# Optimization experiments

Measured on AMD Instinct MI355X. Metric: run time of the kernel, lower is better.

## Reference

```python
import jax, jax.numpy as jnp
import numpy as np

# LLRDenoiser config (init_kwargs): ndim=2, patch W=8, stride S=4, ths=0.1, rand_shift=False
P = 8      # patch size (isotropic)
STRIDE = 4 # patch stride
THS = 0.1  # soft-threshold on singular values
B, C, H, W = 2, 16, 512, 512  # batch, coefficient axis, spatial dims


def setup_inputs() -> dict:
    key = jax.random.key(0)
    x = jax.random.normal(key, (B, C, H, W), dtype=jnp.float32)
    return {"x": x}


def _patch_idx(n, p, s):
    # start indices for sliding windows, inclusive of last full window
    starts = jnp.arange(0, n - p + 1, s)
    return starts[:, None] + jnp.arange(p)[None, :]  # (n_patches, p)


def _llr_denoise(x):
    idx_h = _patch_idx(H, P, STRIDE)  # (nH, P)
    idx_w = _patch_idx(W, P, STRIDE)  # (nW, P)
    nH, nW = idx_h.shape[0], idx_w.shape[0]
    hi = idx_h[:, None, :, None]  # (nH, 1, P, 1)
    wi = idx_w[None, :, None, :]  # (1, nW, 1, P)

    # extract overlapping patches -> (B, C, nH, nW, P, P)
    patches = x[:, :, hi, wi]
    # Casorati matrices per patch: (B, nH*nW, C, P*P)
    mats = patches.transpose(0, 2, 3, 1, 4, 5).reshape(B, nH * nW, C, P * P)

    # batched thin SVD + soft-threshold of singular values
    u, s, vh = jnp.linalg.svd(mats, full_matrices=False)
    s_st = jnp.sign(s) * jnp.maximum(jnp.abs(s) - THS, 0.0)
    mats = (u * s_st[..., None, :]) @ vh

    # back to patch layout (B, C, nH, nW, P, P)
    patches = mats.reshape(B, nH, nW, C, P, P).transpose(0, 3, 1, 2, 4, 5)

    # overlap-add reconstruction, averaged by patch coverage count
    out = jnp.zeros_like(x).at[:, :, hi, wi].add(patches)
    cnt = jnp.zeros((H, W), x.dtype).at[hi[..., 0, :, :] if False else idx_h[:, None, :, None], idx_w[None, :, None, :]].add(1.0)
    return out / cnt


def reference(x):
    return _llr_denoise(x)
```

## Files before the change

### kernel.cpp

```cpp
#include <hip/hip_runtime.h>


#define NBATCH  2
#define NCH     16
#define HDIM    512
#define WDIM    512
#define NPH     127
#define NPW     127
#define NPATCH  (NBATCH * NPH * NPW)
#define NCELL   128
#define THS     0.1f
#define NSIT    8

typedef short bf16x8 __attribute__((ext_vector_type(8)));
typedef float f32x4  __attribute__((ext_vector_type(4)));

#define MFMA(a,b,c) __builtin_amdgcn_mfma_f32_16x16x32_bf16((a),(b),(c),0,0,0)

static __device__ inline short f2bf(float x) {
  return __builtin_bit_cast(short, (__bf16)x);
}
static __device__ inline float blo2f(unsigned int v) {
  return __builtin_bit_cast(float, v << 16);
}
static __device__ inline float bhi2f(unsigned int v) {
  return __builtin_bit_cast(float, v & 0xffff0000u);
}
static __device__ inline unsigned int pack2bf(float lo, float hi) {
  unsigned int a = (unsigned short)f2bf(lo);
  unsigned int b = (unsigned short)f2bf(hi);
  return (b << 16) | a;
}

static __device__ inline int xcd_swz(int b, int nwg) {
  const int q = nwg >> 3, r = nwg & 7;
  const int x = b & 7, lo = b >> 3;
  return (x < r ? x * (q + 1) : r * (q + 1) + (x - r) * q) + lo;
}

static __device__ inline bf16x8 fragc(f32x4 v) {
  bf16x8 r;
  r[0] = f2bf(v[0]); r[1] = f2bf(v[1]); r[2] = f2bf(v[2]); r[3] = f2bf(v[3]);
  r[4] = 0; r[5] = 0; r[6] = 0; r[7] = 0;
  return r;
}

#define ZS_NBLK ((NPATCH + 3) / 4)
__global__ __launch_bounds__(256) void llr_zs(const float* __restrict__ x,
                                              uint2* __restrict__ zs) {
  const int blk = xcd_swz(blockIdx.x, ZS_NBLK);
  const int pid = blk * 4 + (threadIdx.x >> 6);
  if (pid >= NPATCH) return;
  const int bi  = pid / (NPH * NPW);
  const int pr  = pid % (NPH * NPW);
  const int ph  = pr / NPW, pw = pr % NPW;
  const int h0  = ph * 4, w0 = pw * 4;
  const int l   = threadIdx.x & 63;
  const int j   = l & 15;
  const int u   = l >> 4;

  const size_t HW = (size_t)HDIM * WDIM;
  const float* xb = x + (size_t)bi * NCH * HW;

  const float* pb = xb + (size_t)j * HW + (size_t)h0 * WDIM + w0;
  const int dh0 = (u >> 1), dw0 = 4 * (u & 1);
  float4 q0 = *(const float4*)(pb + (size_t)(dh0 + 0) * WDIM + dw0);
  float4 q1 = *(const float4*)(pb + (size_t)(dh0 + 2) * WDIM + dw0);
  float4 q2 = *(const float4*)(pb + (size_t)(dh0 + 4) * WDIM + dw0);
  float4 q3 = *(const float4*)(pb + (size_t)(dh0 + 6) * WDIM + dw0);

  bf16x8 m0, m1;
  m0[0]=f2bf(q0.x); m0[1]=f2bf(q0.y); m0[2]=f2bf(q0.z); m0[3]=f2bf(q0.w);
  m0[4]=f2bf(q1.x); m0[5]=f2bf(q1.y); m0[6]=f2bf(q1.z); m0[7]=f2bf(q1.w);
  m1[0]=f2bf(q2.x); m1[1]=f2bf(q2.y); m1[2]=f2bf(q2.z); m1[3]=f2bf(q2.w);
  m1[4]=f2bf(q3.x); m1[5]=f2bf(q3.y); m1[6]=f2bf(q3.z); m1[7]=f2bf(q3.w);

  f32x4 g = {0.f, 0.f, 0.f, 0.f};
  g = MFMA(m0, m0, g);
  g = MFMA(m1, m1, g);

  float s2 = g[0]*g[0] + g[1]*g[1] + g[2]*g[2] + g[3]*g[3];
  #pragma unroll
  for (int m = 32; m >= 1; m >>= 1) s2 += __shfl_xor(s2, m, 64);

  uint2 wv = {0u, 0u};
  if (s2 > 1e-20f) {
    const float invf  = rsqrtf(s2);
    const float gsc   = 2.0f * invf;
    const float alpha = THS * sqrtf(gsc);

    f32x4 Yc, Zc;
    #pragma unroll
    for (int r = 0; r < 4; ++r) {
      Yc[r] = g[r] * gsc;
      Zc[r] = (4 * u + r == j) ? 1.0f : 0.0f;
    }

    const f32x4 zero = {0.f, 0.f, 0.f, 0.f};
    for (int it = 0; it < NSIT - 1; ++it) {
      bf16x8 yF = fragc(Yc), zF = fragc(Zc);
      f32x4 t  = MFMA(zF, yF, zero);
      bf16x8 tF = fragc(t);
      f32x4 py = MFMA(yF, tF, zero);
      f32x4 pz = MFMA(tF, zF, zero);
      #pragma unroll
      for (int r = 0; r < 4; ++r) {
        Yc[r] = 1.5f * Yc[r] - 0.5f * py[r];
        Zc[r] = 1.5f * Zc[r] - 0.5f * pz[r];
      }
    }
    {
      bf16x8 yF = fragc(Yc), zF = fragc(Zc);
      f32x4 t  = MFMA(zF, yF, zero);
      bf16x8 tF = fragc(t);
      f32x4 pz = MFMA(tF, zF, zero);
      #pragma unroll
      for (int r = 0; r < 4; ++r) Zc[r] = 1.5f * Zc[r] - 0.5f * pz[r];
    }

    wv.x = pack2bf(alpha * Zc[0], alpha * Zc[1]);
    wv.y = pack2bf(alpha * Zc[2], alpha * Zc[3]);
  }
  zs[(size_t)pid * 64 + l] = wv;
}

#define ST_SEG  8
#define ST_NBLK (NBATCH * NCELL * ST_SEG)
__global__ __launch_bounds__(256, 8) void llr_strip(const float* __restrict__ x,
                                                    const uint2* __restrict__ zs,
                                                    float* __restrict__ out) {
  __shared__ unsigned int RS[17 * 132];

  const int bid = blockIdx.x;
  const int seg = bid & 7;
  const int ci  = (bid >> 3) & 127;
  const int bi  = bid >> 10;
  const int t   = threadIdx.x;
  const int r   = t >> 6;
  const int l   = t & 63;

  const size_t HW = (size_t)HDIM * WDIM;
  const float* xb = x + (size_t)bi * NCH * HW;
  float* ob = out + (size_t)bi * NCH * HW;

  const int h   = 4 * ci + r;
  const int wpx = seg * 64 + l;
  const float* px = xb + (size_t)h * WDIM + wpx;
  float xv[16];
  #pragma unroll
  for (int e = 0; e < 16; ++e) xv[e] = px[(size_t)e * HW];

  {
    const int u = l >> 4, j = l & 15;
    const uint2* zb = zs + (size_t)bi * NPH * NPW * 64;
    const bool vh0 = (ci > 0), vh1 = (ci < NPH);
    const int ph0c = vh0 ? ci - 1 : 0;
    const int ph1c = vh1 ? ci : NPH - 1;
    for (int s = r; s < 17; s += 4) {
      const int pw = seg * 16 - 1 + s;
      const bool vw = ((unsigned)pw <= (unsigned)(NPW - 1));
      const int pwc = vw ? pw : 0;
      uint2 z0 = zb[((size_t)ph0c * NPW + pwc) * 64 + l];
      uint2 z1 = zb[((size_t)ph1c * NPW + pwc) * 64 + l];
      if (!(vw && vh0)) { z0.x = 0u; z0.y = 0u; }
      if (!(vw && vh1)) { z1.x = 0u; z1.y = 0u; }
      const float a0 = blo2f(z0.x) + blo2f(z1.x);
      const float a1 = bhi2f(z0.x) + bhi2f(z1.x);
      const float a2 = blo2f(z0.y) + blo2f(z1.y);
      const float a3 = bhi2f(z0.y) + bhi2f(z1.y);
      RS[s * 132 + 32 * u + j]      = pack2bf(a0, a1);
      RS[s * 132 + 32 * u + 16 + j] = pack2bf(a2, a3);
    }
  }
  __syncthreads();

  const int cl = l >> 2;
  const int cj = seg * 16 + cl;
  const float cnth = 2.0f - (ci == 0) - (ci == NCELL - 1);
  const float cntw = 2.0f - (cj == 0) - (cj == NCELL - 1);
  const float sc = 1.0f / (cnth * cntw);

  float* po = ob + (size_t)h * WDIM + wpx;
  #pragma unroll
  for (int p = 0; p < 8; ++p) {
    float d0 = 0.f, d1 = 0.f;
    #pragma unroll
    for (int k = 0; k < 4; ++k) {
      const uint4 A = *(const uint4*)&RS[cl * 132 + 16 * p + 4 * k];
      const uint4 B = *(const uint4*)&RS[(cl + 1) * 132 + 16 * p + 4 * k];
      const unsigned int aa[4] = {A.x, A.y, A.z, A.w};
      const unsigned int bb[4] = {B.x, B.y, B.z, B.w};
      #pragma unroll
      for (int c = 0; c < 4; ++c) {
        const int e = 4 * k + c;
        const float wlo = blo2f(aa[c]) + blo2f(bb[c]);
        const float whi = bhi2f(aa[c]) + bhi2f(bb[c]);
        d0 += wlo * xv[e];
        d1 += whi * xv[e];
      }
    }
    po[(size_t)(2 * p) * HW]     = xv[2 * p]     - sc * d0;
    po[(size_t)(2 * p + 1) * HW] = xv[2 * p + 1] - sc * d1;
  }
}

extern "C" void kernel_launch(void* const* d_in, const int* in_sizes, int n_in,
                              void* d_out, int out_size, void* d_ws, size_t ws_size,
                              hipStream_t stream) {
  const float* x = (const float*)d_in[0];
  float* out = (float*)d_out;
  uint2* zs = (uint2*)d_ws;

  llr_zs<<<dim3(ZS_NBLK), dim3(256), 0, stream>>>(x, zs);
  llr_strip<<<dim3(ST_NBLK), dim3(256), 0, stream>>>(x, zs, out);
}
```

Baseline: 49.99 us.

## Process full cell-row per block with float4 pixel vectorization in strip kernel

The strip kernel now has one 512-thread block cover a whole 4-row cell strip across the full width, instead of eight 64-pixel segments. Each block stages all 129 patch-column weight sets in LDS, about 68KB. Each thread handles one cell (4 pixels) using float4 loads and stores, so the summed 16x16 weight matrix is reused across 4 pixels and LDS traffic per pixel drops. The cost is far fewer blocks (256), much larger LDS use and more registers per thread, which limit occupancy and latency hiding.

```diff
diff --git a/kernel.cpp b/kernel.cpp
--- a/kernel.cpp
+++ b/kernel.cpp
@@ -124,31 +124,22 @@
   zs[(size_t)pid * 64 + l] = wv;
 }
 
-#define ST_SEG  8
-#define ST_NBLK (NBATCH * NCELL * ST_SEG)
-__global__ __launch_bounds__(256, 8) void llr_strip(const float* __restrict__ x,
+#define ST_NBLK (NBATCH * NCELL)
+__global__ __launch_bounds__(512, 2) void llr_strip(const float* __restrict__ x,
                                                     const uint2* __restrict__ zs,
                                                     float* __restrict__ out) {
-  __shared__ unsigned int RS[17 * 132];
+  __shared__ unsigned int RS[129 * 132];
 
   const int bid = blockIdx.x;
-  const int seg = bid & 7;
-  const int ci  = (bid >> 3) & 127;
-  const int bi  = bid >> 10;
+  const int ci  = bid & 127;
+  const int bi  = bid >> 7;
   const int t   = threadIdx.x;
-  const int r   = t >> 6;
+  const int w8  = t >> 6;
   const int l   = t & 63;
 
   const size_t HW = (size_t)HDIM * WDIM;
   const float* xb = x + (size_t)bi * NCH * HW;
   float* ob = out + (size_t)bi * NCH * HW;
-
-  const int h   = 4 * ci + r;
-  const int wpx = seg * 64 + l;
-  const float* px = xb + (size_t)h * WDIM + wpx;
-  float xv[16];
-  #pragma unroll
-  for (int e = 0; e < 16; ++e) xv[e] = px[(size_t)e * HW];
 
   {
     const int u = l >> 4, j = l & 15;
@@ -156,9 +147,9 @@
     const bool vh0 = (ci > 0), vh1 = (ci < NPH);
     const int ph0c = vh0 ? ci - 1 : 0;
     const int ph1c = vh1 ? ci : NPH - 1;
-    for (int s = r; s < 17; s += 4) {
-      const int pw = seg * 16 - 1 + s;
-      const bool vw = ((unsigned)pw <= (unsigned)(NPW - 1));
+    for (int s = w8; s < 129; s += 8) {
+      const int pw = s - 1;
+      const bool vw = ((unsigned)pw <= (unsigned)(NPW - 2));
       const int pwc = vw ? pw : 0;
       uint2 z0 = zb[((size_t)ph0c * NPW + pwc) * 64 + l];
       uint2 z1 = zb[((size_t)ph1c * NPW + pwc) * 64 + l];
@@ -174,20 +165,28 @@
   }
   __syncthreads();
 
-  const int cl = l >> 2;
-  const int cj = seg * 16 + cl;
+  const int r = t >> 7;
+  const int q = t & 127;
+  const int h = 4 * ci + r;
+
+  const float* px = xb + (size_t)h * WDIM + 4 * q;
+  float4 xv[16];
+  #pragma unroll
+  for (int e = 0; e < 16; ++e) xv[e] = *(const float4*)(px + (size_t)e * HW);
+
   const float cnth = 2.0f - (ci == 0) - (ci == NCELL - 1);
-  const float cntw = 2.0f - (cj == 0) - (cj == NCELL - 1);
+  const float cntw = 2.0f - (q == 0) - (q == NCELL - 1);
   const float sc = 1.0f / (cnth * cntw);
 
-  float* po = ob + (size_t)h * WDIM + wpx;
+  float* po = ob + (size_t)h * WDIM + 4 * q;
   #pragma unroll
   for (int p = 0; p < 8; ++p) {
-    float d0 = 0.f, d1 = 0.f;
+    float4 d0 = {0.f, 0.f, 0.f, 0.f};
+    float4 d1 = {0.f, 0.f, 0.f, 0.f};
     #pragma unroll
     for (int k = 0; k < 4; ++k) {
-      const uint4 A = *(const uint4*)&RS[cl * 132 + 16 * p + 4 * k];
-      const uint4 B = *(const uint4*)&RS[(cl + 1) * 132 + 16 * p + 4 * k];
+      const uint4 A = *(const uint4*)&RS[q * 132 + 16 * p + 4 * k];
+      const uint4 B = *(const uint4*)&RS[(q + 1) * 132 + 16 * p + 4 * k];
       const unsigned int aa[4] = {A.x, A.y, A.z, A.w};
       const unsigned int bb[4] = {B.x, B.y, B.z, B.w};
       #pragma unroll
@@ -195,12 +194,20 @@
         const int e = 4 * k + c;
         const float wlo = blo2f(aa[c]) + blo2f(bb[c]);
         const float whi = bhi2f(aa[c]) + bhi2f(bb[c]);
-        d0 += wlo * xv[e];
-        d1 += whi * xv[e];
+        d0.x += wlo * xv[e].x; d0.y += wlo * xv[e].y;
+        d0.z += wlo * xv[e].z; d0.w += wlo * xv[e].w;
+        d1.x += whi * xv[e].x; d1.y += whi * xv[e].y;
+        d1.z += whi * xv[e].z; d1.w += whi * xv[e].w;
       }
     }
-    po[(size_t)(2 * p) * HW]     = xv[2 * p]     - sc * d0;
-    po[(size_t)(2 * p + 1) * HW] = xv[2 * p + 1] - sc * d1;
+    const int c0 = 2 * p, c1 = 2 * p + 1;
+    float4 o0, o1;
+    o0.x = xv[c0].x - sc * d0.x; o0.y = xv[c0].y - sc * d0.y;
+    o0.z = xv[c0].z - sc * d0.z; o0.w = xv[c0].w - sc * d0.w;
+    o1.x = xv[c1].x - sc * d1.x; o1.y = xv[c1].y - sc * d1.y;
+    o1.z = xv[c1].z - sc * d1.z; o1.w = xv[c1].w - sc * d1.w;
+    *(float4*)(po + (size_t)c0 * HW) = o0;
+    *(float4*)(po + (size_t)c1 * HW) = o1;
   }
 }
 
@@ -212,5 +219,5 @@
   uint2* zs = (uint2*)d_ws;
 
   llr_zs<<<dim3(ZS_NBLK), dim3(256), 0, stream>>>(x, zs);
-  llr_strip<<<dim3(ST_NBLK), dim3(256), 0, stream>>>(x, zs, out);
-}
+  llr_strip<<<dim3(ST_NBLK), dim3(512), 0, stream>>>(x, zs, out);
+}
```

New measurement: 47.12 us. 1.06x faster.

## Apply per-cell projection with MFMA in registers instead of LDS-staged scalar dot products

Applied to the files above, without the earlier changes.

The second kernel drops its shared-memory staging of the summed patch weights and the scalar 16-channel dot-product loop. Each wave now loads the neighbouring patch weights straight into registers, combines and scales them per 4x4 cell, and applies the 16x16 channel mixing with one bf16 MFMA per cell. This removes LDS traffic, the block barrier and most of the FMA work. The cost is extra rounding, since x is now rounded to bf16 inside the product, and global loads and stores become scalar, 4-wide per row rather than fully coalesced 64-wide rows, which may hurt memory efficiency.

```diff
diff --git a/kernel.cpp b/kernel.cpp
--- a/kernel.cpp
+++ b/kernel.cpp
@@ -124,83 +124,74 @@
   zs[(size_t)pid * 64 + l] = wv;
 }
 
-#define ST_SEG  8
-#define ST_NBLK (NBATCH * NCELL * ST_SEG)
-__global__ __launch_bounds__(256, 8) void llr_strip(const float* __restrict__ x,
+#define AP_NBLK (NBATCH * NCELL * 8)
+__global__ __launch_bounds__(256, 8) void llr_cells(const float* __restrict__ x,
                                                     const uint2* __restrict__ zs,
                                                     float* __restrict__ out) {
-  __shared__ unsigned int RS[17 * 132];
-
   const int bid = blockIdx.x;
-  const int seg = bid & 7;
+  const int wq  = bid & 7;
   const int ci  = (bid >> 3) & 127;
   const int bi  = bid >> 10;
   const int t   = threadIdx.x;
-  const int r   = t >> 6;
+  const int w   = t >> 6;
   const int l   = t & 63;
+  const int u   = l >> 4, j = l & 15;
 
   const size_t HW = (size_t)HDIM * WDIM;
-  const float* xb = x + (size_t)bi * NCH * HW;
-  float* ob = out + (size_t)bi * NCH * HW;
-
-  const int h   = 4 * ci + r;
-  const int wpx = seg * 64 + l;
-  const float* px = xb + (size_t)h * WDIM + wpx;
-  float xv[16];
+  const int c0  = wq * 16 + w * 4;
+  const int row = 4 * ci + (j >> 2);
+
+  const uint2* zb = zs + (size_t)bi * NPH * NPW * 64;
+  const bool vh0 = (ci > 0), vh1 = (ci < NPH);
+  const int ph0c = vh0 ? ci - 1 : 0;
+  const int ph1c = vh1 ? ci : 0;
+  uint2 s0[5], s1[5];
+  float vws[5];
   #pragma unroll
-  for (int e = 0; e < 16; ++e) xv[e] = px[(size_t)e * HW];
-
-  {
-    const int u = l >> 4, j = l & 15;
-    const uint2* zb = zs + (size_t)bi * NPH * NPW * 64;
-    const bool vh0 = (ci > 0), vh1 = (ci < NPH);
-    const int ph0c = vh0 ? ci - 1 : 0;
-    const int ph1c = vh1 ? ci : NPH - 1;
-    for (int s = r; s < 17; s += 4) {
-      const int pw = seg * 16 - 1 + s;
-      const bool vw = ((unsigned)pw <= (unsigned)(NPW - 1));
-      const int pwc = vw ? pw : 0;
-      uint2 z0 = zb[((size_t)ph0c * NPW + pwc) * 64 + l];
-      uint2 z1 = zb[((size_t)ph1c * NPW + pwc) * 64 + l];
-      if (!(vw && vh0)) { z0.x = 0u; z0.y = 0u; }
-      if (!(vw && vh1)) { z1.x = 0u; z1.y = 0u; }
-      const float a0 = blo2f(z0.x) + blo2f(z1.x);
-      const float a1 = bhi2f(z0.x) + bhi2f(z1.x);
-      const float a2 = blo2f(z0.y) + blo2f(z1.y);
-      const float a3 = bhi2f(z0.y) + bhi2f(z1.y);
-      RS[s * 132 + 32 * u + j]      = pack2bf(a0, a1);
-      RS[s * 132 + 32 * u + 16 + j] = pack2bf(a2, a3);
-    }
+  for (int s = 0; s < 5; ++s) {
+    const int pw = c0 - 1 + s;
+    const bool v = ((unsigned)pw <= (unsigned)(NPW - 1));
+    const int pwc = v ? pw : 0;
+    uint2 a = zb[((size_t)ph0c * NPW + pwc) * 64 + l];
+    uint2 b = zb[((size_t)ph1c * NPW + pwc) * 64 + l];
+    if (!(v && vh0)) { a.x = 0u; a.y = 0u; }
+    if (!(v && vh1)) { b.x = 0u; b.y = 0u; }
+    s0[s] = a; s1[s] = b;
+    vws[s] = v ? 1.0f : 0.0f;
   }
-  __syncthreads();
-
-  const int cl = l >> 2;
-  const int cj = seg * 16 + cl;
   const float cnth = 2.0f - (ci == 0) - (ci == NCELL - 1);
-  const float cntw = 2.0f - (cj == 0) - (cj == NCELL - 1);
-  const float sc = 1.0f / (cnth * cntw);
-
-  float* po = ob + (size_t)h * WDIM + wpx;
+
+  const float* xbse = x + (size_t)bi * NCH * HW + (size_t)(4 * u) * HW
+                        + (size_t)row * WDIM + 4 * c0 + (j & 3);
+  float* obse = out + (size_t)bi * NCH * HW + (size_t)(4 * u) * HW
+                    + (size_t)row * WDIM + 4 * c0 + (j & 3);
+  const f32x4 zero = {0.f, 0.f, 0.f, 0.f};
+
   #pragma unroll
-  for (int p = 0; p < 8; ++p) {
-    float d0 = 0.f, d1 = 0.f;
-    #pragma unroll
-    for (int k = 0; k < 4; ++k) {
-      const uint4 A = *(const uint4*)&RS[cl * 132 + 16 * p + 4 * k];
-      const uint4 B = *(const uint4*)&RS[(cl + 1) * 132 + 16 * p + 4 * k];
-      const unsigned int aa[4] = {A.x, A.y, A.z, A.w};
-      const unsigned int bb[4] = {B.x, B.y, B.z, B.w};
-      #pragma unroll
-      for (int c = 0; c < 4; ++c) {
-        const int e = 4 * k + c;
-        const float wlo = blo2f(aa[c]) + blo2f(bb[c]);
-        const float whi = bhi2f(aa[c]) + bhi2f(bb[c]);
-        d0 += wlo * xv[e];
-        d1 += whi * xv[e];
-      }
-    }
-    po[(size_t)(2 * p) * HW]     = xv[2 * p]     - sc * d0;
-    po[(size_t)(2 * p + 1) * HW] = xv[2 * p + 1] - sc * d1;
+  for (int c = 0; c < 4; ++c) {
+    const float cntw = vws[c] + vws[c + 1];
+    const float sc = 1.0f / (cnth * cntw);
+    f32x4 Wc;
+    Wc[0] = sc * (blo2f(s0[c].x) + blo2f(s1[c].x) + blo2f(s0[c+1].x) + blo2f(s1[c+1].x));
+    Wc[1] = sc * (bhi2f(s0[c].x) + bhi2f(s1[c].x) + bhi2f(s0[c+1].x) + bhi2f(s1[c+1].x));
+    Wc[2] = sc * (blo2f(s0[c].y) + blo2f(s1[c].y) + blo2f(s0[c+1].y) + blo2f(s1[c+1].y));
+    Wc[3] = sc * (bhi2f(s0[c].y) + bhi2f(s1[c].y) + bhi2f(s0[c+1].y) + bhi2f(s1[c+1].y));
+    bf16x8 wF = fragc(Wc);
+
+    float xf0 = xbse[4 * c];
+    float xf1 = xbse[4 * c + HW];
+    float xf2 = xbse[4 * c + 2 * HW];
+    float xf3 = xbse[4 * c + 3 * HW];
+    bf16x8 xF;
+    xF[0] = f2bf(xf0); xF[1] = f2bf(xf1); xF[2] = f2bf(xf2); xF[3] = f2bf(xf3);
+    xF[4] = 0; xF[5] = 0; xF[6] = 0; xF[7] = 0;
+
+    f32x4 d = MFMA(wF, xF, zero);
+
+    obse[4 * c]          = xf0 - d[0];
+    obse[4 * c + HW]     = xf1 - d[1];
+    obse[4 * c + 2 * HW] = xf2 - d[2];
+    obse[4 * c + 3 * HW] = xf3 - d[3];
   }
 }
 
@@ -212,5 +203,5 @@
   uint2* zs = (uint2*)d_ws;
 
   llr_zs<<<dim3(ZS_NBLK), dim3(256), 0, stream>>>(x, zs);
-  llr_strip<<<dim3(ST_NBLK), dim3(256), 0, stream>>>(x, zs, out);
-}
+  llr_cells<<<dim3(AP_NBLK), dim3(256), 0, stream>>>(x, zs, out);
+}
```

Result: faster. 47.38 us (-5.2%).

## Widen strip kernel tiles to 128 columns and stage fp32 weights in LDS

Applied to the files above, without the earlier changes.

Replaces the 64-column strip kernel with a 512-thread block covering a 4x128 pixel tile. Each block now stages 33 patch columns of summed weights instead of 17, which cuts the halo re-reads of the patch-weight buffer. The staged weights are stored as fp32 in a transposed layout, so the inner loop does plain float4 LDS reads and no bf16 unpacking. The cost is more LDS per block (about 34 KB), which can lower occupancy, and each block now covers half as many columns' worth of blocks overall.

```diff
diff --git a/kernel.cpp b/kernel.cpp
--- a/kernel.cpp
+++ b/kernel.cpp
@@ -124,83 +124,76 @@
   zs[(size_t)pid * 64 + l] = wv;
 }
 
-#define ST_SEG  8
-#define ST_NBLK (NBATCH * NCELL * ST_SEG)
-__global__ __launch_bounds__(256, 8) void llr_strip(const float* __restrict__ x,
-                                                    const uint2* __restrict__ zs,
-                                                    float* __restrict__ out) {
-  __shared__ unsigned int RS[17 * 132];
+#define Q_NBLK (NBATCH * NCELL * 4)
+__global__ __launch_bounds__(512, 8) void llr_q(const float* __restrict__ x,
+                                                const uint2* __restrict__ zs,
+                                                float* __restrict__ out) {
+  __shared__ float RS[33 * 260];
 
   const int bid = blockIdx.x;
-  const int seg = bid & 7;
-  const int ci  = (bid >> 3) & 127;
-  const int bi  = bid >> 10;
+  const int qs  = bid & 3;
+  const int ci  = (bid >> 2) & 127;
+  const int bi  = bid >> 9;
   const int t   = threadIdx.x;
-  const int r   = t >> 6;
-  const int l   = t & 63;
+  const int r   = t >> 7;
+  const int px  = t & 127;
+  const int c   = px >> 2;
 
   const size_t HW = (size_t)HDIM * WDIM;
-  const float* xb = x + (size_t)bi * NCH * HW;
-  float* ob = out + (size_t)bi * NCH * HW;
-
   const int h   = 4 * ci + r;
-  const int wpx = seg * 64 + l;
-  const float* px = xb + (size_t)h * WDIM + wpx;
+  const int wpx = qs * 128 + px;
+  const float* xp = x + (size_t)bi * NCH * HW + (size_t)h * WDIM + wpx;
+
   float xv[16];
   #pragma unroll
-  for (int e = 0; e < 16; ++e) xv[e] = px[(size_t)e * HW];
+  for (int e = 0; e < 16; ++e) xv[e] = xp[(size_t)e * HW];
 
   {
-    const int u = l >> 4, j = l & 15;
+    const int w8 = t >> 6;
+    const int l  = t & 63;
+    const int u  = l >> 4, j = l & 15;
     const uint2* zb = zs + (size_t)bi * NPH * NPW * 64;
     const bool vh0 = (ci > 0), vh1 = (ci < NPH);
     const int ph0c = vh0 ? ci - 1 : 0;
     const int ph1c = vh1 ? ci : NPH - 1;
-    for (int s = r; s < 17; s += 4) {
-      const int pw = seg * 16 - 1 + s;
+    for (int s = w8; s < 33; s += 8) {
+      const int pw = qs * 32 - 1 + s;
       const bool vw = ((unsigned)pw <= (unsigned)(NPW - 1));
       const int pwc = vw ? pw : 0;
       uint2 z0 = zb[((size_t)ph0c * NPW + pwc) * 64 + l];
       uint2 z1 = zb[((size_t)ph1c * NPW + pwc) * 64 + l];
       if (!(vw && vh0)) { z0.x = 0u; z0.y = 0u; }
       if (!(vw && vh1)) { z1.x = 0u; z1.y = 0u; }
-      const float a0 = blo2f(z0.x) + blo2f(z1.x);
-      const float a1 = bhi2f(z0.x) + bhi2f(z1.x);
-      const float a2 = blo2f(z0.y) + blo2f(z1.y);
-      const float a3 = bhi2f(z0.y) + bhi2f(z1.y);
-      RS[s * 132 + 32 * u + j]      = pack2bf(a0, a1);
-      RS[s * 132 + 32 * u + 16 + j] = pack2bf(a2, a3);
+      float* rs = &RS[s * 260 + j];
+      rs[16 * (4 * u + 0)] = blo2f(z0.x) + blo2f(z1.x);
+      rs[16 * (4 * u + 1)] = bhi2f(z0.x) + bhi2f(z1.x);
+      rs[16 * (4 * u + 2)] = blo2f(z0.y) + blo2f(z1.y);
+      rs[16 * (4 * u + 3)] = bhi2f(z0.y) + bhi2f(z1.y);
     }
   }
   __syncthreads();
 
-  const int cl = l >> 2;
-  const int cj = seg * 16 + cl;
+  const int cj = qs * 32 + c;
   const float cnth = 2.0f - (ci == 0) - (ci == NCELL - 1);
   const float cntw = 2.0f - (cj == 0) - (cj == NCELL - 1);
   const float sc = 1.0f / (cnth * cntw);
 
-  float* po = ob + (size_t)h * WDIM + wpx;
+  const float* rsA = &RS[c * 260];
+  const float* rsB = &RS[(c + 1) * 260];
+  float* po = out + (size_t)bi * NCH * HW + (size_t)h * WDIM + wpx;
   #pragma unroll
-  for (int p = 0; p < 8; ++p) {
-    float d0 = 0.f, d1 = 0.f;
+  for (int co = 0; co < 16; ++co) {
+    float acc = 0.f;
     #pragma unroll
     for (int k = 0; k < 4; ++k) {
-      const uint4 A = *(const uint4*)&RS[cl * 132 + 16 * p + 4 * k];
-      const uint4 B = *(const uint4*)&RS[(cl + 1) * 132 + 16 * p + 4 * k];
-      const unsigned int aa[4] = {A.x, A.y, A.z, A.w};
-      const unsigned int bb[4] = {B.x, B.y, B.z, B.w};
-      #pragma unroll
-      for (int c = 0; c < 4; ++c) {
-        const int e = 4 * k + c;
-        const float wlo = blo2f(aa[c]) + blo2f(bb[c]);
-        const float whi = bhi2f(aa[c]) + bhi2f(bb[c]);
-        d0 += wlo * xv[e];
-        d1 += whi * xv[e];
-      }
-    }
-    po[(size_t)(2 * p) * HW]     = xv[2 * p]     - sc * d0;
-    po[(size_t)(2 * p + 1) * HW] = xv[2 * p + 1] - sc * d1;
+      const float4 A = *(const float4*)(rsA + 16 * co + 4 * k);
+      const float4 B = *(const float4*)(rsB + 16 * co + 4 * k);
+      acc += (A.x + B.x) * xv[4 * k + 0];
+      acc += (A.y + B.y) * xv[4 * k + 1];
+      acc += (A.z + B.z) * xv[4 * k + 2];
+      acc += (A.w + B.w) * xv[4 * k + 3];
+    }
+    po[(size_t)co * HW] = xv[co] - sc * acc;
   }
 }
 
@@ -212,5 +205,5 @@
   uint2* zs = (uint2*)d_ws;
 
   llr_zs<<<dim3(ZS_NBLK), dim3(256), 0, stream>>>(x, zs);
-  llr_strip<<<dim3(ST_NBLK), dim3(256), 0, stream>>>(x, zs, out);
-}
+  llr_q<<<dim3(Q_NBLK), dim3(512), 0, stream>>>(x, zs, out);
+}
```

New measurement: 48.54 us. 2.9% less time.
